# Kernel tuning notes

Measured on AMD Instinct MI355X. Metric: run time of the kernel, lower is better.

The kernel has to match this reference:

```python
import jax, jax.numpy as jnp
import numpy as np

# SSD Detect post-processing constants (match init_kwargs)
NUM_CLASSES = 21
TOP_K = 200
CONF_THRESH = 0.95
NMS_THRESH = 0.45
M_CAND = 600      # candidate cap; chosen so all boxes passing CONF_THRESH fit (~437 expected)
NEG = -1e30


def setup_inputs() -> dict:
    key = jax.random.key(0)
    k1, k2, k3 = jax.random.split(key, 3)
    B, P, C = 8, 8732, NUM_CLASSES
    loc_data = jax.random.normal(k1, (B, P, 4), dtype=jnp.float32)
    conf_data = jax.random.uniform(k2, (B, P, C), dtype=jnp.float32)
    prior_data = jax.random.uniform(k3, (1, P, 4), dtype=jnp.float32)
    return {"loc_data": loc_data, "conf_data": conf_data, "prior_data": prior_data}


def _nms_lane(boxes_all, scores):
    """One (batch, class) lane. boxes_all: [P,4], scores: [P]. Returns [TOP_K, 5]."""
    pass_mask = scores > CONF_THRESH                       # [P]
    masked = jnp.where(pass_mask, scores, jnp.float32(NEG))
    vals, idx = jax.lax.top_k(masked, M_CAND)              # score-desc candidates (prior idx)
    valid = vals > jnp.float32(NEG / 2)                    # passed threshold
    cb = boxes_all[idx]                                    # [M,4] (x1,y1,x2,y2)
    x1, y1, x2, y2 = cb[:, 0], cb[:, 1], cb[:, 2], cb[:, 3]
    area = (x2 - x1) * (y2 - y1)                           # torchvision-style, no clamp
    xx1 = jnp.maximum(x1[:, None], x1[None, :])
    yy1 = jnp.maximum(y1[:, None], y1[None, :])
    xx2 = jnp.minimum(x2[:, None], x2[None, :])
    yy2 = jnp.minimum(y2[:, None], y2[None, :])
    inter = jnp.clip(xx2 - xx1, 0.0) * jnp.clip(yy2 - yy1, 0.0)
    iou = inter / (area[:, None] + area[None, :] - inter)  # [M,M]
    ar = jnp.arange(M_CAND)

    def body(i, supp):
        keep_i = valid[i] & jnp.logical_not(supp[i])
        return supp | (keep_i & (iou[i] > NMS_THRESH) & (ar > i))

    supp = jax.lax.fori_loop(0, M_CAND, body, jnp.zeros((M_CAND,), bool))
    keep = valid & jnp.logical_not(supp)
    order = jnp.argsort(jnp.logical_not(keep))             # stable: kept first, score order
    n = jnp.minimum(keep.sum(), TOP_K)                     # number of kept boxes (<= TOP_K)
    sel_prior = idx[order[:TOP_K]]                         # prior ids of kept (score order)
    slot_valid = jnp.arange(TOP_K) < n
    fp = jnp.argmax(pass_mask)                             # first prior passing threshold
    prior_ids = jnp.where(slot_valid, sel_prior, fp)       # pad with boxes[0] like torch
    out_scores = jnp.where(slot_valid, scores[prior_ids], 0.0)
    out = jnp.concatenate([out_scores[:, None], boxes_all[prior_ids]], axis=1)  # [K,5]
    return jnp.where(pass_mask.any(), out, jnp.zeros_like(out))


def _forward(loc_data, conf_data, prior_data):
    # prior_data is accepted per the torch signature but unused by the forward math.
    per_batch = jax.vmap(
        lambda boxes, conf_b: jax.vmap(lambda s: _nms_lane(boxes, s))(conf_b[:, 1:].T)
    )
    out_fg = per_batch(loc_data, conf_data)                # [B, C-1, K, 5]
    bg = jnp.zeros_like(out_fg[:, :1])                     # background class row stays 0
    return jnp.concatenate([bg, out_fg], axis=1)           # [B, C, K, 5]


def reference(loc_data, conf_data, prior_data):
    return _forward(loc_data, conf_data, prior_data)
```

## Files before the change

kernel.cpp:

```cpp
#include <hip/hip_runtime.h>
#include <float.h>
#include <math.h>


#define P_PRIORS  8732
#define C_CLASSES 21
#define B_BATCH   8
#define TOPK      200
#define MCAND     600
#define CONF_T    0.95f
#define NMS_T     0.45f
#define NB        64
#define MINB      0x3F733334u

__device__ __forceinline__ uint64_t pack_key(float sc, int p) {
    return ((uint64_t)__float_as_uint(sc) << 32) | (uint32_t)(~(uint32_t)p);
}
__device__ __forceinline__ int bucket_of(uint64_t key) {
    unsigned d = (unsigned)(key >> 32) - MINB;
    int b = (int)(d >> 14);
    return b < (NB - 1) ? b : (NB - 1);
}

#define IOU_ROW(BI, AI, MW, DIAG) do {                                   \
    float xx1 = fmaxf((BI).x, bj.x);                                     \
    float yy1 = fmaxf((BI).y, bj.y);                                     \
    float xx2 = fminf((BI).z, bj.z);                                     \
    float yy2 = fminf((BI).w, bj.w);                                     \
    float ww  = fmaxf(xx2 - xx1, 0.0f);                                  \
    float hh  = fmaxf(yy2 - yy1, 0.0f);                                  \
    float inter = ww * hh;                                               \
    float den   = ((AI) + aj) - inter;              \
    float iou   = inter / den;               \
    uint64_t m = __ballot(iou > NMS_T);                                  \
    if (k == c) m &= (DIAG);                                             \
    (MW) = (lid == k) ? m : (MW);                                        \
} while (0)

__device__ __forceinline__ void iou_rows15(
    int c, int w15, int lid, int M, int kend,
    const float4* s_jb, const float* s_area, uint64_t* s_bm)
{
    const int base = (c << 6);
    const int r0 = base + (w15 - 1);
    const int r1 = r0 + 15, r2 = r0 + 30, r3 = r0 + 45;
    const bool has5 = (w15 <= 4);
    const int r4 = base + 59 + w15;
    const float4 b0 = s_jb[r0], b1 = s_jb[r1], b2 = s_jb[r2], b3 = s_jb[r3];
    const float  a0 = s_area[r0], a1 = s_area[r1], a2 = s_area[r2], a3 = s_area[r3];
    const float4 b4 = s_jb[has5 ? r4 : r0];
    const float  a4 = s_area[has5 ? r4 : r0];
    const uint64_t d0 = ~0ull << (w15);
    const uint64_t d1 = ~0ull << (w15 + 15);
    const uint64_t d2 = ~0ull << (w15 + 30);
    const uint64_t d3 = ~0ull << (w15 + 45);
    const uint64_t d4 = (59 + w15 == 63) ? 0ull : (~0ull << (60 + w15));
    uint64_t w0 = 0, w1 = 0, w2 = 0, w3 = 0, w4 = 0;
    for (int k = c; k < kend; ++k) {
        const float4 bj = s_jb[(k << 6) + lid];
        const float  aj = s_area[(k << 6) + lid];
        IOU_ROW(b0, a0, w0, d0);
        IOU_ROW(b1, a1, w1, d1);
        IOU_ROW(b2, a2, w2, d2);
        IOU_ROW(b3, a3, w3, d3);
        if (has5) { IOU_ROW(b4, a4, w4, d4); }
    }
    if (lid >= c && lid < kend) {
        if (r0 < M) s_bm[(size_t)r0 * 10 + lid] = w0;
        if (r1 < M) s_bm[(size_t)r1 * 10 + lid] = w1;
        if (r2 < M) s_bm[(size_t)r2 * 10 + lid] = w2;
        if (r3 < M) s_bm[(size_t)r3 * 10 + lid] = w3;
        if (has5 && r4 < M) s_bm[(size_t)r4 * 10 + lid] = w4;
    }
}

__global__ __launch_bounds__(1024) void detect_one(
    const float* __restrict__ loc, const float* __restrict__ conf,
    float* __restrict__ out)
{
    const int b   = blockIdx.x & 7;
    const int cls = blockIdx.x >> 3;
    const int tid = threadIdx.x;
    float* o = out + ((size_t)(b * C_CLASSES + cls)) * TOPK * 5;

    if (cls == 0) {
        for (int k = tid; k < TOPK * 5; k += 1024) o[k] = 0.0f;
        return;
    }

    const float*  confb = conf + (size_t)b * P_PRIORS * C_CLASSES + cls;
    const float4* loc4  = (const float4*)(loc + (size_t)b * P_PRIORS * 4);

    __shared__ uint64_t s_bm[MCAND * 10];
    __shared__ float4   s_jb[640];
    __shared__ float    s_area[640];
    __shared__ float    s_ssc[MCAND];
    __shared__ int      s_bcnt[NB], s_bcur[NB], s_boff[NB];
    __shared__ int      s_cnt, s_fp;
    __shared__ uint64_t s_suppw[10], s_keepw[10];
    __shared__ int      s_prefix[10], s_n, s_mstop, s_done;

    uint64_t* s_k   = s_bm;
    uint64_t* s_g   = s_bm + 1024;
    uint64_t* s_srt = s_bm + 2048;

    if (tid < NB)                    s_bcnt[tid] = 0;
    else if (tid < 2 * NB)           s_bcur[tid - NB] = 0;
    else if (tid == 2 * NB)        { s_cnt = 0; s_fp = 0x7FFFFFFF; }
    __syncthreads();

    {
        const int lid = tid & 63;
        float vcur  = confb[(size_t)tid * C_CLASSES];
        float vnext = confb[(size_t)(tid + 1024) * C_CLASSES];
        #pragma unroll
        for (int r = 0; r < 9; ++r) {
            float v = vcur;
            vcur = vnext;
            if (r + 2 <= 7) {
                vnext = confb[(size_t)(tid + ((r + 2) << 10)) * C_CLASSES];
            } else if (r + 2 == 8) {
                int pn = tid + 8192;
                vnext = (pn < P_PRIORS) ? confb[(size_t)pn * C_CLASSES] : 0.0f;
            } else {
                vnext = 0.0f;
            }
            int p = tid + (r << 10);
            bool pass = v > CONF_T;
            uint64_t mask = __ballot(pass);
            if (mask != 0) {
                int leader = (int)__ffsll((unsigned long long)mask) - 1;
                int base = 0;
                if (lid == leader) {
                    base = atomicAdd(&s_cnt, __popcll(mask));
                    atomicMin(&s_fp, p);
                }
                base = __shfl(base, leader, 64);
                if (pass) {
                    int pos = base + __popcll(mask & ((1ull << lid) - 1ull));
                    if (pos < 1024) s_k[pos] = pack_key(v, p);
                }
            }
        }
    }
    __syncthreads();
    int cnt = s_cnt; if (cnt > 1024) cnt = 1024;
    if (cnt == 0) {
        for (int k = tid; k < TOPK * 5; k += 1024) o[k] = 0.0f;
        return;
    }

    for (int t = tid; t < cnt; t += 1024)
        atomicAdd(&s_bcnt[bucket_of(s_k[t])], 1);
    __syncthreads();

    if (tid < 64) {
        int c = s_bcnt[63 - tid];
        int incl = c;
        #pragma unroll
        for (int d = 1; d < 64; d <<= 1) {
            int u = __shfl_up(incl, d, 64);
            if (tid >= d) incl += u;
        }
        s_boff[63 - tid] = incl - c;
    }
    __syncthreads();

    for (int t = tid; t < cnt; t += 1024) {
        uint64_t kt = s_k[t];
        int bb = bucket_of(kt);
        s_g[s_boff[bb] + atomicAdd(&s_bcur[bb], 1)] = kt;
    }
    __syncthreads();

    const int M = cnt < MCAND ? cnt : MCAND;
    {
        const int wid = tid >> 6, lid = tid & 63;
        for (int bb = wid; bb < NB; bb += 16) {
            int st = s_boff[bb], n = s_bcnt[bb];
            for (int e = lid; e < n; e += 64) {
                uint64_t kq = s_g[st + e];
                int r = st;
                for (int q = 0; q < n; ++q)
                    r += (s_g[st + q] > kq) ? 1 : 0;
                if (r < MCAND) s_srt[r] = kq;
            }
        }
    }
    __syncthreads();

    for (int i = tid; i < M; i += 1024) {
        uint64_t key = s_srt[i];
        int p = (int)(~(uint32_t)key);
        s_ssc[i]  = __uint_as_float((uint32_t)(key >> 32));
        float4 bx = loc4[p];
        s_jb[i]   = bx;
        s_area[i] = (bx.z - bx.x) * (bx.w - bx.y);
    }
    for (int i = M + tid; i < 640; i += 1024) {
        s_jb[i]   = make_float4(INFINITY, INFINITY, INFINITY, INFINITY);
        s_area[i] = INFINITY;
    }
    const int fp = s_fp;
    __syncthreads();

    const int kmax = (M + 63) >> 6;
    const int kcap = kmax < 5 ? kmax : 5;

    {
        const int wid = tid >> 6, lid = tid & 63;
        const int w   = (lid < 10) ? lid : 0;
        uint64_t supp = 0;
        int kept = 0, mstop = M;
        const int nch = kcap;

        if (wid > 0) iou_rows15(0, wid, lid, M, kcap, s_jb, s_area, s_bm);
        __syncthreads();

        for (int c = 0; c < nch; ++c) {
            if (wid == 0) {
                const int ibeg = c << 6;
                const int iend = min(ibeg + 64, M);
                uint64_t rb[8];
                #pragma unroll
                for (int d = 0; d < 8; ++d) {
                    int i = ibeg + d;
                    rb[d] = (i < iend) ? s_bm[(size_t)i * 10 + w] : 0;
                }
                for (int i = ibeg; i < iend; ++i) {
                    uint64_t row = rb[i & 7];
                    if (w < c) row = 0;
                    int ip = i + 8;
                    rb[i & 7] = (ip < iend) ? s_bm[(size_t)ip * 10 + w] : 0;
                    bool mybit = (w == c) && ((supp >> (i & 63)) & 1ull);
                    if (!__any((int)mybit)) {
                        supp |= row;
                        if (++kept == TOPK) { mstop = i + 1; break; }
                    }
                }
                if (lid == 0) s_done = (kept >= TOPK) ? 1 : 0;
            } else if (c + 1 < nch) {
                iou_rows15(c + 1, wid, lid, M, kcap, s_jb, s_area, s_bm);
            }
            __syncthreads();
            if (s_done) break;
        }
        if (wid == 0) {
            if (lid < 10) s_suppw[lid] = supp;
            if (lid == 0) s_mstop = mstop;
        }
    }
    __syncthreads();

    if (s_done == 0 && M > 320) {
        const int wid = tid >> 6, lid = tid & 63;
        for (int i = wid; i < M; i += 16) {
            float4 bi = s_jb[i];
            float  ai = s_area[i];
            const int k0 = i >> 6;
            uint64_t diag = ((i & 63) == 63) ? 0ull : (~0ull << ((i & 63) + 1));
            uint64_t myw = 0;
            for (int k = k0; k < kmax; ++k) {
                float4 bj = s_jb[(k << 6) + lid];
                float  aj = s_area[(k << 6) + lid];
                float xx1 = fmaxf(bi.x, bj.x);
                float yy1 = fmaxf(bi.y, bj.y);
                float xx2 = fminf(bi.z, bj.z);
                float yy2 = fminf(bi.w, bj.w);
                float ww  = fmaxf(xx2 - xx1, 0.0f);
                float hh  = fmaxf(yy2 - yy1, 0.0f);
                float inter = ww * hh;
                float den   = (ai + aj) - inter;
                float iou   = inter / den;
                uint64_t m = __ballot(iou > NMS_T);
                if (k == k0) m &= diag;
                myw = (lid == k) ? m : myw;
            }
            if (lid >= k0 && lid < kmax) s_bm[(size_t)i * 10 + lid] = myw;
        }
        __syncthreads();
        if (tid < 64) {
            const int w = (tid < 10) ? tid : 0;
            uint64_t supp = 0;
            int kept = 0, ms = M;
            for (int i = 0; i < M; ++i) {
                uint64_t row = s_bm[(size_t)i * 10 + w];
                if (w < (i >> 6)) row = 0;
                unsigned part  = (unsigned)(supp >> (i & 32));
                unsigned wordv = (unsigned)__builtin_amdgcn_readlane((int)part, i >> 6);
                if (!((wordv >> (i & 31)) & 1u)) {
                    supp |= row;
                    if (++kept == TOPK) { ms = i + 1; break; }
                }
            }
            if (tid < 10) s_suppw[tid] = supp;
            if (tid == 0) s_mstop = ms;
        }
        __syncthreads();
    }

    if (tid == 0) {
        const int Me = s_mstop;
        int total = 0;
        for (int w = 0; w < 10; ++w) {
            uint64_t kw = 0;
            int rem = Me - (w << 6);
            if (rem > 0) {
                uint64_t vm = (rem >= 64) ? ~0ull : ((1ull << rem) - 1ull);
                kw = (~s_suppw[w]) & vm;
            }
            s_keepw[w]  = kw;
            s_prefix[w] = total;
            total += __popcll(kw);
        }
        s_n = total < TOPK ? total : TOPK;
    }
    __syncthreads();

    const int n  = s_n;
    const int Me = s_mstop;
    float4 fbox = loc4[fp];
    for (int k = tid; k < TOPK; k += 1024) {
        if (k >= n) {
            o[k * 5 + 0] = 0.0f;
            o[k * 5 + 1] = fbox.x; o[k * 5 + 2] = fbox.y;
            o[k * 5 + 3] = fbox.z; o[k * 5 + 4] = fbox.w;
        }
    }
    for (int t = tid; t < Me; t += 1024) {
        uint64_t kw = s_keepw[t >> 6];
        if ((kw >> (t & 63)) & 1ull) {
            int r = s_prefix[t >> 6] + __popcll(kw & ((1ull << (t & 63)) - 1ull));
            if (r < TOPK) {
                float4 bx = s_jb[t];
                o[r * 5 + 0] = s_ssc[t];
                o[r * 5 + 1] = bx.x; o[r * 5 + 2] = bx.y;
                o[r * 5 + 3] = bx.z; o[r * 5 + 4] = bx.w;
            }
        }
    }
}

extern "C" void kernel_launch(void* const* d_in, const int* in_sizes, int n_in,
                              void* d_out, int out_size, void* d_ws, size_t ws_size,
                              hipStream_t stream) {
    const float* loc  = (const float*)d_in[0];
    const float* conf = (const float*)d_in[1];
    float* out = (float*)d_out;
    (void)d_ws; (void)ws_size;

    detect_one<<<dim3(B_BATCH * C_CLASSES), dim3(1024), 0, stream>>>(loc, conf, out);
}
```

Baseline: 103.8 us.

## Fuse sort scatter with box gather and precompute first IoU chunk with all warps

The rank-sort pass now writes score, box and area straight into their sorted slots, which removes the intermediate sorted-key buffer and one block barrier. The first 64-row IoU bitmask chunk is now computed by all 16 warps through a new 4-rows-per-warp routine instead of 15 warps. The pipelined chunk cap drops from 5 to 4, so more lanes may fall back to the full-matrix path when about 437 candidates pass the threshold. This trades fewer speculative chunks against a higher chance of running the slower fallback path.

```diff
diff --git a/kernel.cpp b/kernel.cpp
--- a/kernel.cpp
+++ b/kernel.cpp
@@ -12,6 +12,7 @@
 #define NMS_T     0.45f
 #define NB        64
 #define MINB      0x3F733334u
+#define KCAP      4
 
 __device__ __forceinline__ uint64_t pack_key(float sc, int p) {
     return ((uint64_t)__float_as_uint(sc) << 32) | (uint32_t)(~(uint32_t)p);
@@ -36,6 +37,36 @@
     if (k == c) m &= (DIAG);                                             \
     (MW) = (lid == k) ? m : (MW);                                        \
 } while (0)
+
+__device__ __forceinline__ void iou_chunk16(
+    int c, int wid, int lid, int M, int kend,
+    const float4* s_jb, const float* s_area, uint64_t* s_bm)
+{
+    const int i0 = (c << 6) + wid;
+    const float4 b0 = s_jb[i0],      b1 = s_jb[i0 + 16],
+                 b2 = s_jb[i0 + 32], b3 = s_jb[i0 + 48];
+    const float  a0 = s_area[i0],      a1 = s_area[i0 + 16],
+                 a2 = s_area[i0 + 32], a3 = s_area[i0 + 48];
+    const uint64_t d0 = ~0ull << (wid + 1);
+    const uint64_t d1 = ~0ull << (wid + 17);
+    const uint64_t d2 = ~0ull << (wid + 33);
+    const uint64_t d3 = (wid == 15) ? 0ull : (~0ull << (wid + 49));
+    uint64_t w0 = 0, w1 = 0, w2 = 0, w3 = 0;
+    for (int k = c; k < kend; ++k) {
+        const float4 bj = s_jb[(k << 6) + lid];
+        const float  aj = s_area[(k << 6) + lid];
+        IOU_ROW(b0, a0, w0, d0);
+        IOU_ROW(b1, a1, w1, d1);
+        IOU_ROW(b2, a2, w2, d2);
+        IOU_ROW(b3, a3, w3, d3);
+    }
+    if (lid >= c && lid < kend) {
+        if (i0      < M) s_bm[(size_t)(i0     ) * 10 + lid] = w0;
+        if (i0 + 16 < M) s_bm[(size_t)(i0 + 16) * 10 + lid] = w1;
+        if (i0 + 32 < M) s_bm[(size_t)(i0 + 32) * 10 + lid] = w2;
+        if (i0 + 48 < M) s_bm[(size_t)(i0 + 48) * 10 + lid] = w3;
+    }
+}
 
 __device__ __forceinline__ void iou_rows15(
     int c, int w15, int lid, int M, int kend,
@@ -100,9 +131,8 @@
     __shared__ uint64_t s_suppw[10], s_keepw[10];
     __shared__ int      s_prefix[10], s_n, s_mstop, s_done;
 
-    uint64_t* s_k   = s_bm;
-    uint64_t* s_g   = s_bm + 1024;
-    uint64_t* s_srt = s_bm + 2048;
+    uint64_t* s_k = s_bm;
+    uint64_t* s_g = s_bm + 1024;
 
     if (tid < NB)                    s_bcnt[tid] = 0;
     else if (tid < 2 * NB)           s_bcur[tid - NB] = 0;
@@ -183,19 +213,15 @@
                 int r = st;
                 for (int q = 0; q < n; ++q)
                     r += (s_g[st + q] > kq) ? 1 : 0;
-                if (r < MCAND) s_srt[r] = kq;
-            }
-        }
-    }
-    __syncthreads();
-
-    for (int i = tid; i < M; i += 1024) {
-        uint64_t key = s_srt[i];
-        int p = (int)(~(uint32_t)key);
-        s_ssc[i]  = __uint_as_float((uint32_t)(key >> 32));
-        float4 bx = loc4[p];
-        s_jb[i]   = bx;
-        s_area[i] = (bx.z - bx.x) * (bx.w - bx.y);
+                if (r < MCAND) {
+                    int p = (int)(~(uint32_t)kq);
+                    s_ssc[r]  = __uint_as_float((uint32_t)(kq >> 32));
+                    float4 bx = loc4[p];
+                    s_jb[r]   = bx;
+                    s_area[r] = (bx.z - bx.x) * (bx.w - bx.y);
+                }
+            }
+        }
     }
     for (int i = M + tid; i < 640; i += 1024) {
         s_jb[i]   = make_float4(INFINITY, INFINITY, INFINITY, INFINITY);
@@ -205,7 +231,7 @@
     __syncthreads();
 
     const int kmax = (M + 63) >> 6;
-    const int kcap = kmax < 5 ? kmax : 5;
+    const int kcap = kmax < KCAP ? kmax : KCAP;
 
     {
         const int wid = tid >> 6, lid = tid & 63;
@@ -214,7 +240,7 @@
         int kept = 0, mstop = M;
         const int nch = kcap;
 
-        if (wid > 0) iou_rows15(0, wid, lid, M, kcap, s_jb, s_area, s_bm);
+        iou_chunk16(0, wid, lid, M, kcap, s_jb, s_area, s_bm);
         __syncthreads();
 
         for (int c = 0; c < nch; ++c) {
@@ -252,7 +278,7 @@
     }
     __syncthreads();
 
-    if (s_done == 0 && M > 320) {
+    if (s_done == 0 && M > (KCAP << 6)) {
         const int wid = tid >> 6, lid = tid & 63;
         for (int i = wid; i < M; i += 16) {
             float4 bi = s_jb[i];
```

New measurement: 100.5 us (median of 3 runs). 1.03x faster.
